# Optimization experiments

Measured on AMD Instinct MI355X. Metric: run time of the kernel, lower is better.

## Reference

```python
import jax, jax.numpy as jnp
import numpy as np

B, L, D = 2, 4096, 1024
NUM_HEADS = 16
HEAD_DIM = D // NUM_HEADS
WINDOW = 256
NUM_EXPERTS = 8
EXPERT_DIM = 1024
FF_HIDDEN = 4096
TOP_K = 2
ENTROPY_WEIGHT = 0.1
BIDIRECTIONAL = True


def layer_norm(x, g, b, eps=1e-5):
    m = x.mean(-1, keepdims=True)
    v = ((x - m) ** 2).mean(-1, keepdims=True)
    return (x - m) * jax.lax.rsqrt(v + eps) * g + b


def local_attention(x, qkv_w, qkv_b, out_w, out_b):
    # Non-overlapping windowed multi-head attention. L % WINDOW == 0 by construction.
    Bx, Lx, Dx = x.shape
    qkv = x @ qkv_w + qkv_b                      # [B,L,3D]
    q, k, v = jnp.split(qkv, 3, axis=-1)
    nw = Lx // WINDOW
    rs = lambda t: t.reshape(Bx, nw, WINDOW, NUM_HEADS, HEAD_DIM)
    q, k, v = rs(q), rs(k), rs(v)
    scale = 1.0 / np.sqrt(HEAD_DIM)
    scores = jnp.einsum('bnqhd,bnkhd->bnhqk', q, k) * scale   # [B,nw,H,W,W]
    if not BIDIRECTIONAL:
        causal = jnp.tril(jnp.ones((WINDOW, WINDOW), bool))
        scores = jnp.where(causal, scores, jnp.asarray(-1e9, scores.dtype))
    attn = jax.nn.softmax(scores, axis=-1)
    o = jnp.einsum('bnhqk,bnkhd->bnqhd', attn, v).reshape(Bx, Lx, Dx)
    return o @ out_w + out_b


def dilated_conv(x, w, b):
    # x: [B,L,D]; w: [D_out, D_in, K=3], dilation=2 -> effective kernel 5, pad 2 keeps length.
    y = jax.lax.conv_general_dilated(
        x.transpose(0, 2, 1), w, window_strides=(1,), padding=[(2, 2)], rhs_dilation=(2,))
    return y.transpose(0, 2, 1) + b


def moe(x, gate_w, gate_b, expert_w, expert_b):
    logits = x @ gate_w + gate_b                 # [B,L,E]
    probs = jax.nn.softmax(logits, axis=-1)
    topv, topi = jax.lax.top_k(probs, TOP_K)
    topv = topv / topv.sum(-1, keepdims=True)
    # combine weights, zero except at the top-k experts
    combine = (jax.nn.one_hot(topi, NUM_EXPERTS, dtype=x.dtype) * topv[..., None]).sum(-2)  # [B,L,E]
    y = jnp.einsum('bld,edf->blef', x, expert_w) + expert_b   # [B,L,E,De]
    out = jnp.einsum('blef,ble->blf', jax.nn.gelu(y, approximate=False), combine)
    entropy = -(probs * jnp.log(probs + 1e-10)).sum(-1).mean()
    return out, ENTROPY_WEIGHT * entropy


def setup_inputs() -> dict:
    key = jax.random.key(0)
    ks = jax.random.split(key, 16)
    s = 0.02
    return {
        'x': jax.random.normal(ks[0], (B, L, D), jnp.float32),
        'ln1_g': jnp.ones((D,), jnp.float32), 'ln1_b': jnp.zeros((D,), jnp.float32),
        'qkv_w': jax.random.normal(ks[1], (D, 3 * D), jnp.float32) * s,
        'qkv_b': jnp.zeros((3 * D,), jnp.float32),
        'attn_out_w': jax.random.normal(ks[2], (D, D), jnp.float32) * s,
        'attn_out_b': jnp.zeros((D,), jnp.float32),
        'ln2_g': jnp.ones((D,), jnp.float32), 'ln2_b': jnp.zeros((D,), jnp.float32),
        'conv_w': jax.random.normal(ks[3], (D, D, 3), jnp.float32) * s,
        'conv_b': jnp.zeros((D,), jnp.float32),
        'ln3_g': jnp.ones((D,), jnp.float32), 'ln3_b': jnp.zeros((D,), jnp.float32),
        'gate_w': jax.random.normal(ks[4], (D, NUM_EXPERTS), jnp.float32) * s,
        'gate_b': jnp.zeros((NUM_EXPERTS,), jnp.float32),
        'expert_w': jax.random.normal(ks[5], (NUM_EXPERTS, D, EXPERT_DIM), jnp.float32) * s,
        'expert_b': jnp.zeros((NUM_EXPERTS, EXPERT_DIM), jnp.float32),
        'ff_w1': jax.random.normal(ks[6], (D, FF_HIDDEN), jnp.float32) * s,
        'ff_b1': jnp.zeros((FF_HIDDEN,), jnp.float32),
        'ff_w2': jax.random.normal(ks[7], (FF_HIDDEN, D), jnp.float32) * s,
        'ff_b2': jnp.zeros((D,), jnp.float32),
    }


def reference(x, ln1_g, ln1_b, qkv_w, qkv_b, attn_out_w, attn_out_b,
              ln2_g, ln2_b, conv_w, conv_b, ln3_g, ln3_b,
              gate_w, gate_b, expert_w, expert_b,
              ff_w1, ff_b1, ff_w2, ff_b2):
    # dropout layers are identity in eval mode
    x = x + local_attention(layer_norm(x, ln1_g, ln1_b), qkv_w, qkv_b, attn_out_w, attn_out_b)
    x = x + dilated_conv(layer_norm(x, ln2_g, ln2_b), conv_w, conv_b)
    moe_out, entropy_loss = moe(layer_norm(x, ln3_g, ln3_b), gate_w, gate_b, expert_w, expert_b)
    x = x + moe_out
    h = jax.nn.gelu(x @ ff_w1 + ff_b1, approximate=False) @ ff_w2 + ff_b2
    x = x + h
    return x, entropy_loss
```

## Files before the change

kernel.cpp:

```cpp
#include <hip/hip_runtime.h>
#include <hip/hip_bf16.h>
#include <math.h>


typedef unsigned short UST;
typedef unsigned int uint32;
typedef float f32x4 __attribute__((ext_vector_type(4)));
using s16x8 = __attribute__((ext_vector_type(8))) short;

#define DEV __device__ __forceinline__
#define MFMA16 __builtin_amdgcn_mfma_f32_16x16x32_bf16

#define GLL(g, l) __builtin_amdgcn_global_load_lds( \
    (const __attribute__((address_space(1))) unsigned int*)(g), \
    (__attribute__((address_space(3))) unsigned int*)(l), 16, 0, 0)

#define BARRIER()  asm volatile("s_barrier" ::: "memory")
#define LGKM0()    asm volatile("s_waitcnt lgkmcnt(0)" ::: "memory")
#define VM0()      asm volatile("s_waitcnt vmcnt(0)" ::: "memory")

DEV UST f2bf(float f) {
    uint32 u = __float_as_uint(f);
    u += 0x7FFFu + ((u >> 16) & 1u);
    return (UST)(u >> 16);
}
DEV float bf2f(UST h) { return __uint_as_float(((uint32)h) << 16); }
DEV float gelu_f(float x) { return 0.5f * x * (1.0f + erff(x * 0.7071067811865475f)); }

__global__ void ln_split_kernel(const float* __restrict__ x,
                                const float* __restrict__ g, const float* __restrict__ b,
                                UST* __restrict__ oh, UST* __restrict__ ol)
{
    const int t = blockIdx.x;
    const int tid = threadIdx.x;
    const float4 v = ((const float4*)(x + (long)t * 1024))[tid];
    float s = v.x + v.y + v.z + v.w;
    float q = v.x * v.x + v.y * v.y + v.z * v.z + v.w * v.w;
    for (int o = 32; o > 0; o >>= 1) { s += __shfl_xor(s, o, 64); q += __shfl_xor(q, o, 64); }
    __shared__ float ss[4], sq[4];
    const int wave = tid >> 6, lane = tid & 63;
    if (lane == 0) { ss[wave] = s; sq[wave] = q; }
    __syncthreads();
    s = ss[0] + ss[1] + ss[2] + ss[3];
    q = sq[0] + sq[1] + sq[2] + sq[3];
    const float mean = s * (1.0f / 1024.0f);
    const float var = q * (1.0f / 1024.0f) - mean * mean;
    const float rstd = 1.0f / sqrtf(var + 1e-5f);
    const long row = (long)t + 2 + 4 * (t >> 12);
    UST* ph = oh + row * 1024 + tid * 4;
    UST* pl = ol + row * 1024 + tid * 4;
    const float4 gg = ((const float4*)g)[tid];
    const float4 bb = ((const float4*)b)[tid];
    float vv[4] = { v.x, v.y, v.z, v.w };
    float gv[4] = { gg.x, gg.y, gg.z, gg.w };
    float bv[4] = { bb.x, bb.y, bb.z, bb.w };
#pragma unroll
    for (int j = 0; j < 4; j++) {
        float f = (vv[j] - mean) * rstd * gv[j] + bv[j];
        UST hi = f2bf(f);
        ph[j] = hi;
        pl[j] = f2bf(f - bf2f(hi));
    }
}

__global__ void ln_pad_kernel(UST* __restrict__ oh, UST* __restrict__ ol)
{
    const int blk = blockIdx.x;
    const int b = blk >> 2, rsel = blk & 3;
    const long row = (long)b * 4100 + (rsel < 2 ? rsel : 4096 + rsel);
    const int tid = threadIdx.x;
    *(ushort4*)(oh + row * 1024 + tid * 4) = make_ushort4(0, 0, 0, 0);
    *(ushort4*)(ol + row * 1024 + tid * 4) = make_ushort4(0, 0, 0, 0);
}

__global__ void prep_t_kernel(const float* __restrict__ src, UST* __restrict__ dh,
                              UST* __restrict__ dl, int N, int K)
{
    __shared__ float tile[32][65];
    const int k0 = blockIdx.y * 32, n0 = blockIdx.x * 64;
    const int t = threadIdx.x;
    const int nn = t & 63, kk = t >> 6;
#pragma unroll
    for (int i = 0; i < 8; i++)
        tile[kk + i * 4][nn] = src[(long)(k0 + kk + i * 4) * N + n0 + nn];
    __syncthreads();
    const int kw = (t & 7) * 4;
#pragma unroll
    for (int pass = 0; pass < 2; pass++) {
        const int nw = (t >> 3) + pass * 32;
        UST hv[4], lv[4];
#pragma unroll
        for (int j = 0; j < 4; j++) {
            float v = tile[kw + j][nw];
            hv[j] = f2bf(v);
            lv[j] = f2bf(v - bf2f(hv[j]));
        }
        UST* bh = dh + (long)(n0 + nw) * K + k0 + kw;
        *(ushort4*)bh = make_ushort4(hv[0], hv[1], hv[2], hv[3]);
        if (dl) {
            UST* bl = dl + (long)(n0 + nw) * K + k0 + kw;
            *(ushort4*)bl = make_ushort4(lv[0], lv[1], lv[2], lv[3]);
        }
    }
}

__global__ void prep_w_kernel(const float* __restrict__ src, UST* __restrict__ dh,
                              UST* __restrict__ dl, int K, long sr, long sc,
                              int dstK, int dstOff, long total)
{
    long gid = (long)blockIdx.x * 256 + threadIdx.x;
    if (gid >= total) return;
    long n = gid / K, k = gid - n * K;
    float v = src[k * sr + n * sc];
    UST hi = f2bf(v);
    long di = n * dstK + dstOff + k;
    dh[di] = hi;
    if (dl) dl[di] = f2bf(v - bf2f(hi));
}

template<int EPI, bool SPLIT, int ASHIFT>
__global__ __launch_bounds__(256)
void gemm_bt_kernel(const UST* __restrict__ Ah, const UST* __restrict__ Al,
                    const UST* __restrict__ Bh, const UST* __restrict__ Bl,
                    const float* __restrict__ bias, const float* __restrict__ resid,
                    float* __restrict__ Cf, UST* __restrict__ Cb, UST* __restrict__ Sp,
                    int M, int N, int K, int KA, int rb, int radd)
{
    constexpr int ABUF = (SPLIT ? 2 : 1) * 4096;
    __shared__ UST sA[2 * ABUF];
    __shared__ UST sB[2 * ABUF];
    const int tid = threadIdx.x;
    const int lane = tid & 63;
    const int wv = __builtin_amdgcn_readfirstlane(tid >> 6);
    const int wr = wv >> 1, wc = wv & 1;
    const int lm = lane & 15, lq = lane >> 4;

    const unsigned nwg = gridDim.x * gridDim.y;
    const unsigned orig = blockIdx.y * gridDim.x + blockIdx.x;
    const unsigned wg = (orig & 7u) * (nwg >> 3) + (orig >> 3);
    const int bx = (int)(wg % gridDim.x), by = (int)(wg / gridDim.x);
    const long m0 = (long)by * 128, n0 = (long)bx * 128;

    const int lr = lane >> 2, lc = (lane & 3) * 8;
    const int rA0 = wv * 32 + lr, rA1 = wv * 32 + 16 + lr;
    const long mtop = m0 >> 12;
    const UST* gA0 = Ah + (m0 + rA0 + rb + (long)radd * mtop) * KA + lc;
    const UST* gA1 = Ah + (m0 + rA1 + rb + (long)radd * mtop) * KA + lc;
    const UST* gB0 = Bh + (n0 + rA0) * K + lc;
    const UST* gB1 = Bh + (n0 + rA1) * K + lc;
    const UST* gA0l = SPLIT ? (Al + (m0 + rA0 + rb + (long)radd * mtop) * KA + lc) : nullptr;
    const UST* gA1l = SPLIT ? (Al + (m0 + rA1 + rb + (long)radd * mtop) * KA + lc) : nullptr;
    const UST* gB0l = SPLIT ? (Bl + (n0 + rA0) * K + lc) : nullptr;
    const UST* gB1l = SPLIT ? (Bl + (n0 + rA1) * K + lc) : nullptr;

    f32x4 acc[4][4] = {};
    s16x8 ah[4], bh[4], al[4], bl[4];

    auto stage = [&](int kk, UST* dA, UST* dB) {
        const long aoff = ASHIFT ? (long)kk + (long)(kk >> 10) * ASHIFT : (long)kk;
        GLL(gA0 + aoff, dA); GLL(gA1 + aoff, dA + 512);
        GLL(gB0 + kk, dB); GLL(gB1 + kk, dB + 512);
        if (SPLIT) {
            GLL(gA0l + aoff, dA + 4096); GLL(gA1l + aoff, dA + 512 + 4096);
            GLL(gB0l + kk, dB + 4096); GLL(gB1l + kk, dB + 512 + 4096);
        }
    };
    auto loads = [&](const UST* cA, const UST* cB) {
#pragma unroll
        for (int i = 0; i < 4; i++) {
            ah[i] = *(const s16x8*)&cA[(wr * 64 + i * 16 + lm) * 32 + lq * 8];
            bh[i] = *(const s16x8*)&cB[(wc * 64 + i * 16 + lm) * 32 + lq * 8];
        }
        if constexpr (SPLIT) {
#pragma unroll
            for (int i = 0; i < 4; i++) {
                al[i] = *(const s16x8*)&cA[4096 + (wr * 64 + i * 16 + lm) * 32 + lq * 8];
                bl[i] = *(const s16x8*)&cB[4096 + (wc * 64 + i * 16 + lm) * 32 + lq * 8];
            }
        }
    };
    auto mfma_all = [&]() {
        __builtin_amdgcn_s_setprio(1);
#pragma unroll
        for (int i = 0; i < 4; i++)
#pragma unroll
            for (int j = 0; j < 4; j++)
                acc[i][j] = MFMA16(ah[i], bh[j], acc[i][j], 0, 0, 0);
        if constexpr (SPLIT) {
#pragma unroll
            for (int i = 0; i < 4; i++)
#pragma unroll
                for (int j = 0; j < 4; j++)
                    acc[i][j] = MFMA16(ah[i], bl[j], acc[i][j], 0, 0, 0);
#pragma unroll
            for (int i = 0; i < 4; i++)
#pragma unroll
                for (int j = 0; j < 4; j++)
                    acc[i][j] = MFMA16(al[i], bh[j], acc[i][j], 0, 0, 0);
        }
        __builtin_amdgcn_s_setprio(0);
    };
    auto vm_cur = [&]() {
        if constexpr (SPLIT) asm volatile("s_waitcnt vmcnt(8)" ::: "memory");
        else                 asm volatile("s_waitcnt vmcnt(4)" ::: "memory");
    };

    UST* wA0 = &sA[wv * 1024];
    UST* wB0 = &sB[wv * 1024];
    UST* wA1 = &sA[ABUF + wv * 1024];
    UST* wB1 = &sB[ABUF + wv * 1024];

    stage(0, wA0, wB0);
    stage(32, wA1, wB1);
    for (int k0 = 0; k0 + 64 < K; k0 += 64) {
        vm_cur(); BARRIER();
        loads(&sA[0], &sB[0]);
        LGKM0(); BARRIER();
        stage(k0 + 64, wA0, wB0);
        mfma_all();
        vm_cur(); BARRIER();
        loads(&sA[ABUF], &sB[ABUF]);
        LGKM0(); BARRIER();
        stage(k0 + 96, wA1, wB1);
        mfma_all();
    }
    vm_cur(); BARRIER();
    loads(&sA[0], &sB[0]);
    mfma_all();
    VM0(); BARRIER();
    loads(&sA[ABUF], &sB[ABUF]);
    mfma_all();

    const long SZ = 8388608L;
    const int colbase = (int)n0 + wc * 64;
    const int part = colbase >> 10;
    const int hh = (colbase & 1023) >> 6;
    UST* H = (EPI == 2) ? (Sp + (long)part * 2 * SZ) : nullptr;
    UST* Lo = (EPI == 2) ? (H + SZ) : nullptr;
#pragma unroll
    for (int i = 0; i < 4; i++) {
#pragma unroll
        for (int j = 0; j < 4; j++) {
#pragma unroll
            for (int r = 0; r < 4; r++) {
                const long grow = m0 + wr * 64 + i * 16 + lq * 4 + r;
                const long gcol = n0 + wc * 64 + j * 16 + lm;
                float v = acc[i][j][r];
                if (bias) v += bias[gcol];
                if (EPI == 0) {
                    const long idx = grow * N + gcol;
                    if (resid) v += resid[idx];
                    Cf[idx] = v;
                } else if (EPI == 1) {
                    Cb[grow * N + gcol] = f2bf(gelu_f(v));
                } else {
                    const int d = j * 16 + lm;
                    long idx;
                    if (part < 2) {
                        idx = ((long)hh * 8192 + grow) * 64 + d;
                    } else {
                        const int bb = (int)(grow >> 12), ww = (int)((grow >> 8) & 15),
                                  tt = (int)(grow & 255);
                        idx = ((long)((bb * 16 + ww) * 16 + hh)) * 16384 + (long)d * 256 + tt;
                    }
                    UST hi = f2bf(v);
                    H[idx] = hi;
                    Lo[idx] = f2bf(v - bf2f(hi));
                }
            }
        }
    }
}

__global__ __launch_bounds__(256, 2)
void attn_mfma_kernel(const UST* __restrict__ Sp, UST* __restrict__ oh, UST* __restrict__ ol)
{
    __shared__ UST sPh[4 * 64 * 40];
    __shared__ UST sPl[4 * 64 * 40];
    const long SZ = 8388608L;
    const UST* Qh = Sp;
    const UST* Ql = Sp + SZ;
    const UST* Kh = Sp + 2 * SZ;
    const UST* Kl = Sp + 3 * SZ;
    const UST* Vth = Sp + 4 * SZ;
    const UST* Vtl = Sp + 5 * SZ;
    const int blk = blockIdx.x;
    const int h = blk & 15, w = (blk >> 4) & 15, b = blk >> 8;
    const long tok0 = (long)b * 4096 + w * 256;
    const int tid = threadIdx.x;
    const int lane = tid & 63;
    const int wv = tid >> 6;
    const int lm = lane & 15, lq = lane >> 4;

    const long qrow0 = (long)h * 8192 + tok0 + wv * 64;
    s16x8 qhf[4][2], qlf[4][2];
#pragma unroll
    for (int mt = 0; mt < 4; mt++)
#pragma unroll
        for (int ks = 0; ks < 2; ks++) {
            const long o = (qrow0 + mt * 16 + lm) * 64 + ks * 32 + lq * 8;
            qhf[mt][ks] = *(const s16x8*)(Qh + o);
            qlf[mt][ks] = *(const s16x8*)(Ql + o);
        }
    const long krow0 = (long)h * 8192 + tok0;
    const long vbase = (long)blk * 16384;

    f32x4 Oacc[4][4] = {};
    float lsum[4][4] = {};
    UST* myPh = &sPh[wv * 2560];
    UST* myPl = &sPl[wv * 2560];

    for (int c = 0; c < 8; c++) {
        const int kt = c * 32;
        f32x4 S[4][2] = {};
#pragma unroll
        for (int nt = 0; nt < 2; nt++)
#pragma unroll
            for (int ks = 0; ks < 2; ks++) {
                const long o = (krow0 + kt + nt * 16 + lm) * 64 + ks * 32 + lq * 8;
                s16x8 khf = *(const s16x8*)(Kh + o);
                s16x8 klf = *(const s16x8*)(Kl + o);
#pragma unroll
                for (int mt = 0; mt < 4; mt++) {
                    S[mt][nt] = MFMA16(qhf[mt][ks], khf, S[mt][nt], 0, 0, 0);
                    S[mt][nt] = MFMA16(qhf[mt][ks], klf, S[mt][nt], 0, 0, 0);
                    S[mt][nt] = MFMA16(qlf[mt][ks], khf, S[mt][nt], 0, 0, 0);
                }
            }
#pragma unroll
        for (int mt = 0; mt < 4; mt++)
#pragma unroll
            for (int r = 0; r < 4; r++) {
                float p0 = __expf(S[mt][0][r] * 0.125f);
                float p1 = __expf(S[mt][1][r] * 0.125f);
                float part = p0 + p1;
                part += __shfl_xor(part, 1, 64);
                part += __shfl_xor(part, 2, 64);
                part += __shfl_xor(part, 4, 64);
                part += __shfl_xor(part, 8, 64);
                lsum[mt][r] += part;
                const int q = mt * 16 + lq * 4 + r;
                UST h0 = f2bf(p0), h1 = f2bf(p1);
                myPh[q * 40 + lm] = h0;
                myPh[q * 40 + 16 + lm] = h1;
                myPl[q * 40 + lm] = f2bf(p0 - bf2f(h0));
                myPl[q * 40 + 16 + lm] = f2bf(p1 - bf2f(h1));
            }
#pragma unroll
        for (int mt = 0; mt < 4; mt++) {
            s16x8 phf = *(const s16x8*)(myPh + (mt * 16 + lm) * 40 + lq * 8);
            s16x8 plf = *(const s16x8*)(myPl + (mt * 16 + lm) * 40 + lq * 8);
#pragma unroll
            for (int dt = 0; dt < 4; dt++) {
                const long o = vbase + (dt * 16 + lm) * 256 + kt + lq * 8;
                s16x8 vhf = *(const s16x8*)(Vth + o);
                s16x8 vlf = *(const s16x8*)(Vtl + o);
                Oacc[mt][dt] = MFMA16(phf, vhf, Oacc[mt][dt], 0, 0, 0);
                Oacc[mt][dt] = MFMA16(phf, vlf, Oacc[mt][dt], 0, 0, 0);
                Oacc[mt][dt] = MFMA16(plf, vhf, Oacc[mt][dt], 0, 0, 0);
            }
        }
    }
#pragma unroll
    for (int mt = 0; mt < 4; mt++)
#pragma unroll
        for (int r = 0; r < 4; r++) {
            const float inv = 1.0f / lsum[mt][r];
            const long tok = tok0 + wv * 64 + mt * 16 + lq * 4 + r;
            UST* po = oh + tok * 1024 + h * 64;
            UST* plo = ol + tok * 1024 + h * 64;
#pragma unroll
            for (int dt = 0; dt < 4; dt++) {
                float f = Oacc[mt][dt][r] * inv;
                UST hv = f2bf(f);
                po[dt * 16 + lm] = hv;
                plo[dt * 16 + lm] = f2bf(f - bf2f(hv));
            }
        }
}

__global__ void gate_kernel(const UST* __restrict__ lnh, const UST* __restrict__ lnl,
                            const float* __restrict__ gw, const float* __restrict__ gb,
                            float* __restrict__ combine, float* __restrict__ ent_acc)
{
    const int tid = threadIdx.x;
    const int t = blockIdx.x * 4 + (tid >> 6);
    const int lane = tid & 63;
    const long row = (long)t + 2 + 4 * (t >> 12);
    const UST* ph = lnh + row * 1024;
    const UST* pl = lnl + row * 1024;
    float acc[8] = { 0, 0, 0, 0, 0, 0, 0, 0 };
    for (int c = 0; c < 16; c++) {
        int d = c * 64 + lane;
        float xv = bf2f(ph[d]) + bf2f(pl[d]);
        const float* wr = gw + (long)d * 8;
#pragma unroll
        for (int e = 0; e < 8; e++) acc[e] += xv * wr[e];
    }
#pragma unroll
    for (int e = 0; e < 8; e++)
        for (int o = 32; o > 0; o >>= 1) acc[e] += __shfl_xor(acc[e], o, 64);
    if (lane == 0) {
        float lg[8], p[8];
        float mx = -1e30f;
        for (int e = 0; e < 8; e++) { lg[e] = acc[e] + gb[e]; mx = fmaxf(mx, lg[e]); }
        float sum = 0;
        for (int e = 0; e < 8; e++) { p[e] = expf(lg[e] - mx); sum += p[e]; }
        float inv = 1.0f / sum;
        float ent = 0;
        for (int e = 0; e < 8; e++) { p[e] *= inv; ent -= p[e] * logf(p[e] + 1e-10f); }
        int i1 = 0; float v1 = -1e30f;
        for (int e = 0; e < 8; e++) if (p[e] > v1) { v1 = p[e]; i1 = e; }
        int i2 = 0; float v2 = -1e30f;
        for (int e = 0; e < 8; e++) if (e != i1 && p[e] > v2) { v2 = p[e]; i2 = e; }
        float inv2 = 1.0f / (v1 + v2);
        float cw[8] = { 0, 0, 0, 0, 0, 0, 0, 0 };
        cw[i1] = v1 * inv2; cw[i2] = v2 * inv2;
        float* co = combine + (long)t * 8;
        for (int e = 0; e < 8; e++) co[e] = cw[e];
        atomicAdd(ent_acc, ent);
    }
}

__global__ void moe_combine_kernel(const UST* __restrict__ y, const float* __restrict__ combine,
                                   float* __restrict__ out, int halfsel)
{
    const long gid = (long)blockIdx.x * 256 + threadIdx.x;
    const int t = (int)(gid >> 10), f = (int)(gid & 1023);
    const float* cw = combine + (long)t * 8 + halfsel * 4;
    const UST* yp = y + (long)t * 4096 + f;
    float s = cw[0] * bf2f(yp[0]) + cw[1] * bf2f(yp[1024])
            + cw[2] * bf2f(yp[2048]) + cw[3] * bf2f(yp[3072]);
    out[gid] += s;
}

__global__ void f32_to_bf16_kernel(const float* __restrict__ in, UST* __restrict__ out)
{
    long gid = ((long)blockIdx.x * 256 + threadIdx.x) * 4;
    float4 v = *(const float4*)(in + gid);
    out[gid] = f2bf(v.x); out[gid + 1] = f2bf(v.y);
    out[gid + 2] = f2bf(v.z); out[gid + 3] = f2bf(v.w);
}

__global__ void ent_final_kernel(const float* __restrict__ acc, float* __restrict__ out)
{
    out[0] = 0.1f * acc[0] * (1.0f / 8192.0f);
}

extern "C" void kernel_launch(void* const* d_in, const int* in_sizes, int n_in,
                              void* d_out_, int out_size, void* d_ws, size_t ws_size,
                              hipStream_t stream)
{
    const float* x      = (const float*)d_in[0];
    const float* ln1_g  = (const float*)d_in[1];
    const float* ln1_b  = (const float*)d_in[2];
    const float* qkv_w  = (const float*)d_in[3];
    const float* qkv_b  = (const float*)d_in[4];
    const float* ao_w   = (const float*)d_in[5];
    const float* ao_b   = (const float*)d_in[6];
    const float* ln2_g  = (const float*)d_in[7];
    const float* ln2_b  = (const float*)d_in[8];
    const float* conv_w = (const float*)d_in[9];
    const float* conv_b = (const float*)d_in[10];
    const float* ln3_g  = (const float*)d_in[11];
    const float* ln3_b  = (const float*)d_in[12];
    const float* gate_w = (const float*)d_in[13];
    const float* gate_b = (const float*)d_in[14];
    const float* exp_w  = (const float*)d_in[15];
    const float* exp_b  = (const float*)d_in[16];
    const float* ff_w1  = (const float*)d_in[17];
    const float* ff_b1  = (const float*)d_in[18];
    const float* ff_w2  = (const float*)d_in[19];
    const float* ff_b2  = (const float*)d_in[20];
    float* out = (float*)d_out_;

    char* ws = (char*)d_ws;
    size_t off = 0;
    auto alloc = [&](size_t bytes) -> char* {
        char* p = ws + off;
        off += (bytes + 255) & ~(size_t)255;
        return p;
    };
    UST* qkvWh = (UST*)alloc(3072 * 1024 * 2);
    UST* qkvWl = (UST*)alloc(3072 * 1024 * 2);
    UST* aoWh  = (UST*)alloc(1024 * 1024 * 2);
    UST* aoWl  = (UST*)alloc(1024 * 1024 * 2);
    UST* convCh = (UST*)alloc(1024L * 3072 * 2);
    UST* convCl = (UST*)alloc(1024L * 3072 * 2);
    UST* expW  = (UST*)alloc(8192L * 1024 * 2);
    UST* ff1W  = (UST*)alloc(4096L * 1024 * 2);
    UST* ff2W  = (UST*)alloc(4096L * 1024 * 2);
    const size_t LN_BYTES = 8200L * 1024 * 2;
    UST* LNh = (UST*)alloc(LN_BYTES);
    UST* LNl = (UST*)alloc(LN_BYTES);
    float* combine = (float*)alloc(8192 * 8 * 4);
    float* entacc  = (float*)alloc(256);
    char*  BIG = alloc(8192L * 3072 * 4);
    UST* OH = (UST*)alloc(8192L * 1024 * 2);
    UST* OL = (UST*)alloc(8192L * 1024 * 2);
    if (off > ws_size) return;

    UST* Sp   = (UST*)BIG;
    UST* ybuf = (UST*)BIG;
    UST* h1   = (UST*)BIG;
    UST* x3h  = OH;

    auto nb = [](long n) { return (unsigned)((n + 255) / 256); };
    prep_t_kernel<<<dim3(48, 32), 256, 0, stream>>>(qkv_w, qkvWh, qkvWl, 3072, 1024);
    prep_t_kernel<<<dim3(16, 32), 256, 0, stream>>>(ao_w, aoWh, aoWl, 1024, 1024);
    for (int k = 0; k < 3; k++)
        prep_w_kernel<<<nb(1024L * 1024), 256, 0, stream>>>(conv_w + k, convCh, convCl,
                                                            1024, 3, 3072, 3072, k * 1024, 1024L * 1024);
    for (int e = 0; e < 8; e++)
        prep_t_kernel<<<dim3(16, 32), 256, 0, stream>>>(exp_w + (long)e * 1048576, expW + (long)e * 1048576,
                                                        nullptr, 1024, 1024);
    prep_t_kernel<<<dim3(64, 32), 256, 0, stream>>>(ff_w1, ff1W, nullptr, 4096, 1024);
    prep_t_kernel<<<dim3(16, 128), 256, 0, stream>>>(ff_w2, ff2W, nullptr, 1024, 4096);

    ln_pad_kernel<<<8, 256, 0, stream>>>(LNh, LNl);
    hipMemsetAsync(entacc, 0, 4, stream);

    ln_split_kernel<<<8192, 256, 0, stream>>>(x, ln1_g, ln1_b, LNh, LNl);
    gemm_bt_kernel<2, true, 0><<<dim3(24, 64), 256, 0, stream>>>(LNh, LNl, qkvWh, qkvWl, qkv_b, nullptr,
                                                                 nullptr, nullptr, Sp, 8192, 3072, 1024, 1024, 2, 4);
    attn_mfma_kernel<<<512, 256, 0, stream>>>(Sp, OH, OL);
    gemm_bt_kernel<0, true, 0><<<dim3(8, 64), 256, 0, stream>>>(OH, OL, aoWh, aoWl, ao_b, x,
                                                                out, nullptr, nullptr, 8192, 1024, 1024, 1024, 0, 0);
    ln_split_kernel<<<8192, 256, 0, stream>>>(out, ln2_g, ln2_b, LNh, LNl);
    gemm_bt_kernel<0, true, 1024><<<dim3(8, 64), 256, 0, stream>>>(LNh, LNl, convCh, convCl, conv_b, out,
                                                                   out, nullptr, nullptr, 8192, 1024, 3072, 1024, 0, 4);
    ln_split_kernel<<<8192, 256, 0, stream>>>(out, ln3_g, ln3_b, LNh, LNl);
    gate_kernel<<<2048, 256, 0, stream>>>(LNh, LNl, gate_w, gate_b, combine, entacc);
    ent_final_kernel<<<1, 1, 0, stream>>>(entacc, out + 8388608);
    for (int hh = 0; hh < 2; hh++) {
        gemm_bt_kernel<1, false, 0><<<dim3(32, 64), 256, 0, stream>>>(LNh, nullptr, expW + (long)hh * 4096 * 1024,
                                                                      nullptr, exp_b + hh * 4096, nullptr,
                                                                      nullptr, ybuf, nullptr, 8192, 4096, 1024, 1024, 2, 4);
        moe_combine_kernel<<<32768, 256, 0, stream>>>(ybuf, combine, out, hh);
    }
    f32_to_bf16_kernel<<<8192, 256, 0, stream>>>(out, x3h);
    gemm_bt_kernel<1, false, 0><<<dim3(32, 64), 256, 0, stream>>>(x3h, nullptr, ff1W, nullptr, ff_b1, nullptr,
                                                                  nullptr, h1, nullptr, 8192, 4096, 1024, 1024, 0, 0);
    gemm_bt_kernel<0, false, 0><<<dim3(8, 64), 256, 0, stream>>>(h1, nullptr, ff2W, nullptr, ff_b2, out,
                                                                 out, nullptr, nullptr, 8192, 1024, 4096, 4096, 0, 0);
}
```

Baseline: 1.410 ms.

## Route MoE tokens to top-2 experts with gathered GEMM and atomic combine

Replaces the dense all-expert MoE GEMM (8 experts computed for every token) with a token-routed grouped GEMM. The gate kernel builds per-expert token lists with atomics, and each GEMM tile gathers its expert's rows and scatter-adds the gelu output times the combine weight into the output. The separate combine kernel is removed. This cuts expert FLOPs roughly fourfold, at the cost of gathered row loads, fp32 atomics in the epilogue with nondeterministic summation order, and a grid sized for a worst-case tile count.

```diff
diff --git a/kernel.cpp b/kernel.cpp
--- a/kernel.cpp
+++ b/kernel.cpp
@@ -118,13 +118,15 @@
     if (dl) dl[di] = f2bf(v - bf2f(hi));
 }
 
-template<int EPI, bool SPLIT, int ASHIFT>
+template<int EPI, bool SPLIT, int ASHIFT, bool GATHER>
 __global__ __launch_bounds__(256)
 void gemm_bt_kernel(const UST* __restrict__ Ah, const UST* __restrict__ Al,
                     const UST* __restrict__ Bh, const UST* __restrict__ Bl,
                     const float* __restrict__ bias, const float* __restrict__ resid,
                     float* __restrict__ Cf, UST* __restrict__ Cb, UST* __restrict__ Sp,
-                    int M, int N, int K, int KA, int rb, int radd)
+                    int M, int N, int K, int KA, int rb, int radd,
+                    const int* __restrict__ cnt8, const int* __restrict__ perm,
+                    const float* __restrict__ combine)
 {
     constexpr int ABUF = (SPLIT ? 2 : 1) * 4096;
     __shared__ UST sA[2 * ABUF];
@@ -135,23 +137,58 @@
     const int wr = wv >> 1, wc = wv & 1;
     const int lm = lane & 15, lq = lane >> 4;
 
-    const unsigned nwg = gridDim.x * gridDim.y;
-    const unsigned orig = blockIdx.y * gridDim.x + blockIdx.x;
-    const unsigned wg = (orig & 7u) * (nwg >> 3) + (orig >> 3);
-    const int bx = (int)(wg % gridDim.x), by = (int)(wg / gridDim.x);
-    const long m0 = (long)by * 128, n0 = (long)bx * 128;
+    int eidx = 0, cnt_e = 0, segbase = 0;
+    long m0, n0;
+    if constexpr (GATHER) {
+        int mt = (int)blockIdx.y;
+        int cnts[8];
+#pragma unroll
+        for (int e2 = 0; e2 < 8; e2++) cnts[e2] = cnt8[e2];
+        int e2 = 0;
+        for (;;) {
+            const int te = (cnts[e2] + 127) >> 7;
+            if (mt < te) break;
+            mt -= te;
+            if (++e2 == 8) return;
+        }
+        eidx = e2; cnt_e = cnts[e2]; segbase = e2 << 13;
+        m0 = (long)mt * 128;
+        n0 = (long)blockIdx.x * 128;
+    } else {
+        const unsigned nwg = gridDim.x * gridDim.y;
+        const unsigned orig = blockIdx.y * gridDim.x + blockIdx.x;
+        const unsigned wg = (orig & 7u) * (nwg >> 3) + (orig >> 3);
+        m0 = (long)(wg / gridDim.x) * 128;
+        n0 = (long)(wg % gridDim.x) * 128;
+    }
 
     const int lr = lane >> 2, lc = (lane & 3) * 8;
     const int rA0 = wv * 32 + lr, rA1 = wv * 32 + 16 + lr;
-    const long mtop = m0 >> 12;
-    const UST* gA0 = Ah + (m0 + rA0 + rb + (long)radd * mtop) * KA + lc;
-    const UST* gA1 = Ah + (m0 + rA1 + rb + (long)radd * mtop) * KA + lc;
-    const UST* gB0 = Bh + (n0 + rA0) * K + lc;
-    const UST* gB1 = Bh + (n0 + rA1) * K + lc;
-    const UST* gA0l = SPLIT ? (Al + (m0 + rA0 + rb + (long)radd * mtop) * KA + lc) : nullptr;
-    const UST* gA1l = SPLIT ? (Al + (m0 + rA1 + rb + (long)radd * mtop) * KA + lc) : nullptr;
-    const UST* gB0l = SPLIT ? (Bl + (n0 + rA0) * K + lc) : nullptr;
-    const UST* gB1l = SPLIT ? (Bl + (n0 + rA1) * K + lc) : nullptr;
+    const UST *gA0, *gA1;
+    const UST *gA0l = nullptr, *gA1l = nullptr, *gB0l = nullptr, *gB1l = nullptr;
+    const UST* Bhe = Bh;
+    if constexpr (GATHER) {
+        const int p0 = (int)m0 + rA0, p1 = (int)m0 + rA1;
+        const int i0 = (p0 < cnt_e) ? perm[segbase + p0] : 0;
+        const int i1 = (p1 < cnt_e) ? perm[segbase + p1] : 0;
+        gA0 = Ah + (long)i0 * KA + lc;
+        gA1 = Ah + (long)i1 * KA + lc;
+        Bhe = Bh + ((long)eidx << 20);
+    } else {
+        const long mtop = m0 >> 12;
+        gA0 = Ah + (m0 + rA0 + rb + (long)radd * mtop) * KA + lc;
+        gA1 = Ah + (m0 + rA1 + rb + (long)radd * mtop) * KA + lc;
+        if constexpr (SPLIT) {
+            gA0l = Al + (m0 + rA0 + rb + (long)radd * mtop) * KA + lc;
+            gA1l = Al + (m0 + rA1 + rb + (long)radd * mtop) * KA + lc;
+        }
+    }
+    const UST* gB0 = Bhe + (n0 + rA0) * K + lc;
+    const UST* gB1 = Bhe + (n0 + rA1) * K + lc;
+    if constexpr (SPLIT) {
+        gB0l = Bl + (n0 + rA0) * K + lc;
+        gB1l = Bl + (n0 + rA1) * K + lc;
+    }
 
     f32x4 acc[4][4] = {};
     s16x8 ah[4], bh[4], al[4], bl[4];
@@ -237,6 +274,8 @@
     const int hh = (colbase & 1023) >> 6;
     UST* H = (EPI == 2) ? (Sp + (long)part * 2 * SZ) : nullptr;
     UST* Lo = (EPI == 2) ? (H + SZ) : nullptr;
+    const float* bias_e = bias;
+    if constexpr (GATHER) bias_e = bias + (eidx << 10);
 #pragma unroll
     for (int i = 0; i < 4; i++) {
 #pragma unroll
@@ -246,13 +285,20 @@
                 const long grow = m0 + wr * 64 + i * 16 + lq * 4 + r;
                 const long gcol = n0 + wc * 64 + j * 16 + lm;
                 float v = acc[i][j][r];
-                if (bias) v += bias[gcol];
+                if (bias) v += bias_e[gcol];
                 if (EPI == 0) {
                     const long idx = grow * N + gcol;
                     if (resid) v += resid[idx];
                     Cf[idx] = v;
                 } else if (EPI == 1) {
                     Cb[grow * N + gcol] = f2bf(gelu_f(v));
+                } else if (EPI == 3) {
+                    if (grow < cnt_e) {
+                        const int prow = perm[segbase + grow];
+                        const int tok = prow - ((prow < 4100) ? 2 : 6);
+                        const float wgt = combine[(long)tok * 8 + eidx];
+                        atomicAdd(&Cf[(long)tok * 1024 + gcol], gelu_f(v) * wgt);
+                    }
                 } else {
                     const int d = j * 16 + lm;
                     long idx;
@@ -381,7 +427,8 @@
 
 __global__ void gate_kernel(const UST* __restrict__ lnh, const UST* __restrict__ lnl,
                             const float* __restrict__ gw, const float* __restrict__ gb,
-                            float* __restrict__ combine, float* __restrict__ ent_acc)
+                            float* __restrict__ combine, float* __restrict__ ent_acc,
+                            int* __restrict__ cnt8, int* __restrict__ perm)
 {
     const int tid = threadIdx.x;
     const int t = blockIdx.x * 4 + (tid >> 6);
@@ -418,20 +465,12 @@
         cw[i1] = v1 * inv2; cw[i2] = v2 * inv2;
         float* co = combine + (long)t * 8;
         for (int e = 0; e < 8; e++) co[e] = cw[e];
+        const int s1 = atomicAdd(&cnt8[i1], 1);
+        perm[(i1 << 13) + s1] = (int)row;
+        const int s2 = atomicAdd(&cnt8[i2], 1);
+        perm[(i2 << 13) + s2] = (int)row;
         atomicAdd(ent_acc, ent);
     }
-}
-
-__global__ void moe_combine_kernel(const UST* __restrict__ y, const float* __restrict__ combine,
-                                   float* __restrict__ out, int halfsel)
-{
-    const long gid = (long)blockIdx.x * 256 + threadIdx.x;
-    const int t = (int)(gid >> 10), f = (int)(gid & 1023);
-    const float* cw = combine + (long)t * 8 + halfsel * 4;
-    const UST* yp = y + (long)t * 4096 + f;
-    float s = cw[0] * bf2f(yp[0]) + cw[1] * bf2f(yp[1024])
-            + cw[2] * bf2f(yp[2048]) + cw[3] * bf2f(yp[3072]);
-    out[gid] += s;
 }
 
 __global__ void f32_to_bf16_kernel(const float* __restrict__ in, UST* __restrict__ out)
@@ -495,13 +534,14 @@
     UST* LNl = (UST*)alloc(LN_BYTES);
     float* combine = (float*)alloc(8192 * 8 * 4);
     float* entacc  = (float*)alloc(256);
+    int*   cnt8    = (int*)alloc(256);
+    int*   perm    = (int*)alloc(8 * 8192 * 4);
     char*  BIG = alloc(8192L * 3072 * 4);
     UST* OH = (UST*)alloc(8192L * 1024 * 2);
     UST* OL = (UST*)alloc(8192L * 1024 * 2);
     if (off > ws_size) return;
 
     UST* Sp   = (UST*)BIG;
-    UST* ybuf = (UST*)BIG;
     UST* h1   = (UST*)BIG;
     UST* x3h  = OH;
 
@@ -519,28 +559,31 @@
 
     ln_pad_kernel<<<8, 256, 0, stream>>>(LNh, LNl);
     hipMemsetAsync(entacc, 0, 4, stream);
+    hipMemsetAsync(cnt8, 0, 32, stream);
 
     ln_split_kernel<<<8192, 256, 0, stream>>>(x, ln1_g, ln1_b, LNh, LNl);
-    gemm_bt_kernel<2, true, 0><<<dim3(24, 64), 256, 0, stream>>>(LNh, LNl, qkvWh, qkvWl, qkv_b, nullptr,
-                                                                 nullptr, nullptr, Sp, 8192, 3072, 1024, 1024, 2, 4);
+    gemm_bt_kernel<2, true, 0, false><<<dim3(24, 64), 256, 0, stream>>>(
+        LNh, LNl, qkvWh, qkvWl, qkv_b, nullptr, nullptr, nullptr, Sp,
+        8192, 3072, 1024, 1024, 2, 4, nullptr, nullptr, nullptr);
     attn_mfma_kernel<<<512, 256, 0, stream>>>(Sp, OH, OL);
-    gemm_bt_kernel<0, true, 0><<<dim3(8, 64), 256, 0, stream>>>(OH, OL, aoWh, aoWl, ao_b, x,
-                                                                out, nullptr, nullptr, 8192, 1024, 1024, 1024, 0, 0);
+    gemm_bt_kernel<0, true, 0, false><<<dim3(8, 64), 256, 0, stream>>>(
+        OH, OL, aoWh, aoWl, ao_b, x, out, nullptr, nullptr,
+        8192, 1024, 1024, 1024, 0, 0, nullptr, nullptr, nullptr);
     ln_split_kernel<<<8192, 256, 0, stream>>>(out, ln2_g, ln2_b, LNh, LNl);
-    gemm_bt_kernel<0, true, 1024><<<dim3(8, 64), 256, 0, stream>>>(LNh, LNl, convCh, convCl, conv_b, out,
-                                                                   out, nullptr, nullptr, 8192, 1024, 3072, 1024, 0, 4);
+    gemm_bt_kernel<0, true, 1024, false><<<dim3(8, 64), 256, 0, stream>>>(
+        LNh, LNl, convCh, convCl, conv_b, out, out, nullptr, nullptr,
+        8192, 1024, 3072, 1024, 0, 4, nullptr, nullptr, nullptr);
     ln_split_kernel<<<8192, 256, 0, stream>>>(out, ln3_g, ln3_b, LNh, LNl);
-    gate_kernel<<<2048, 256, 0, stream>>>(LNh, LNl, gate_w, gate_b, combine, entacc);
+    gate_kernel<<<2048, 256, 0, stream>>>(LNh, LNl, gate_w, gate_b, combine, entacc, cnt8, perm);
     ent_final_kernel<<<1, 1, 0, stream>>>(entacc, out + 8388608);
-    for (int hh = 0; hh < 2; hh++) {
-        gemm_bt_kernel<1, false, 0><<<dim3(32, 64), 256, 0, stream>>>(LNh, nullptr, expW + (long)hh * 4096 * 1024,
-                                                                      nullptr, exp_b + hh * 4096, nullptr,
-                                                                      nullptr, ybuf, nullptr, 8192, 4096, 1024, 1024, 2, 4);
-        moe_combine_kernel<<<32768, 256, 0, stream>>>(ybuf, combine, out, hh);
-    }
+    gemm_bt_kernel<3, false, 0, true><<<dim3(8, 136), 256, 0, stream>>>(
+        LNh, nullptr, expW, nullptr, exp_b, nullptr, out, nullptr, nullptr,
+        8192, 1024, 1024, 1024, 0, 0, cnt8, perm, combine);
     f32_to_bf16_kernel<<<8192, 256, 0, stream>>>(out, x3h);
-    gemm_bt_kernel<1, false, 0><<<dim3(32, 64), 256, 0, stream>>>(x3h, nullptr, ff1W, nullptr, ff_b1, nullptr,
-                                                                  nullptr, h1, nullptr, 8192, 4096, 1024, 1024, 0, 0);
-    gemm_bt_kernel<0, false, 0><<<dim3(8, 64), 256, 0, stream>>>(h1, nullptr, ff2W, nullptr, ff_b2, out,
-                                                                 out, nullptr, nullptr, 8192, 1024, 4096, 4096, 0, 0);
-}
+    gemm_bt_kernel<1, false, 0, false><<<dim3(32, 64), 256, 0, stream>>>(
+        x3h, nullptr, ff1W, nullptr, ff_b1, nullptr, nullptr, h1, nullptr,
+        8192, 4096, 1024, 1024, 0, 0, nullptr, nullptr, nullptr);
+    gemm_bt_kernel<0, false, 0, false><<<dim3(8, 64), 256, 0, stream>>>(
+        h1, nullptr, ff2W, nullptr, ff_b2, out, out, nullptr, nullptr,
+        8192, 1024, 4096, 4096, 0, 0, nullptr, nullptr, nullptr);
+}
```

Result: faster. 1.359 ms (-3.6%).
